# Optimization experiments

Hardware: AMD Instinct MI355X
Metric: run time of the kernel (lower is better)

Reference implementation:

```python
import jax, jax.numpy as jnp
import numpy as np

EMB, HEADS, LAT, FFN = 1024, 16, 256, 4096
HD = EMB // HEADS
B, N = 2, 2048

def _ln(x, w, b, eps=1e-5):
    mu = jnp.mean(x, axis=-1, keepdims=True)
    var = jnp.var(x, axis=-1, keepdims=True)
    return (x - mu) * jax.lax.rsqrt(var + eps) * w + b

def setup_inputs() -> dict:
    key = jax.random.key(0)
    ks = jax.random.split(key, 16)
    def lin(k, fan_in, fan_out):
        bound = 1.0 / np.sqrt(fan_in)
        kw, kb = jax.random.split(k)
        W = jax.random.uniform(kw, (fan_in, fan_out), jnp.float32, -bound, bound)
        b = jax.random.uniform(kb, (fan_out,), jnp.float32, -bound, bound)
        return W, b
    Wq, bq = lin(ks[0], EMB, EMB)
    WaK, baK = lin(ks[1], EMB, LAT)
    WbK, bbK = lin(ks[2], LAT, EMB)
    WaV, baV = lin(ks[3], EMB, LAT)
    WbV, bbV = lin(ks[4], LAT, EMB)
    Wo, bo = lin(ks[5], EMB, EMB)
    W1, b1 = lin(ks[6], EMB, FFN)
    W2, b2 = lin(ks[7], FFN, EMB)
    return {
        'x': jax.random.normal(ks[8], (B, N, EMB), jnp.float32),
        'attn_bias': jax.random.normal(ks[9], (N, N), jnp.float32),
        'Wq': Wq, 'bq': bq, 'WaK': WaK, 'baK': baK, 'WbK': WbK, 'bbK': bbK,
        'WaV': WaV, 'baV': baV, 'WbV': WbV, 'bbV': bbV, 'Wo': Wo, 'bo': bo,
        'W1': W1, 'b1': b1, 'W2': W2, 'b2': b2,
        'ln1_w': jnp.ones((EMB,), jnp.float32), 'ln1_b': jnp.zeros((EMB,), jnp.float32),
        'ln2_w': jnp.ones((EMB,), jnp.float32), 'ln2_b': jnp.zeros((EMB,), jnp.float32),
    }

def reference(x, attn_bias, Wq, bq, WaK, baK, WbK, bbK, WaV, baV, WbV, bbV,
              Wo, bo, W1, b1, W2, b2, ln1_w, ln1_b, ln2_w, ln2_b):
    Q = x @ Wq + bq                       # [B,N,E]
    K = (x @ WaK + baK) @ WbK + bbK       # low-rank K
    V = (x @ WaV + baV) @ WbV + bbV       # low-rank V
    def split(t):
        return t.reshape(B, N, HEADS, HD).transpose(0, 2, 1, 3)  # [B,H,N,D]
    Qh, Kh, Vh = split(Q), split(K), split(V)
    scores = jnp.einsum('bhnd,bhmd->bhnm', Qh, Kh) / np.sqrt(HD)
    scores = scores + attn_bias[None, None]
    weights = jax.nn.softmax(scores, axis=-1)
    attn = jnp.einsum('bhnm,bhmd->bhnd', weights, Vh)
    attn = attn.transpose(0, 2, 1, 3).reshape(B, N, EMB)
    attn = attn @ Wo + bo
    h = _ln(x + attn, ln1_w, ln1_b)
    ffn = jax.nn.gelu(h @ W1 + b1, approximate=False) @ W2 + b2
    return _ln(h + ffn, ln2_w, ln2_b)
```

## Files before the change

### kernel.cpp

```cpp
#include <hip/hip_runtime.h>
#include <hip/hip_bf16.h>
#include <math.h>

typedef unsigned short u16;
typedef short bf16x8 __attribute__((ext_vector_type(8)));
typedef float f32x4 __attribute__((ext_vector_type(4)));

#define EMB   1024
#define HEADS 16
#define HD    64
#define LATD  256
#define FFND  4096
#define BATCH 2
#define SEQ   2048
#define TOK   (BATCH*SEQ)

#define SCL2  0.18033688011112042f
#define LOG2E 1.4426950408889634f

__device__ __forceinline__ float bf2f(u16 u) {
    union { unsigned int i; float f; } x; x.i = ((unsigned int)u) << 16; return x.f;
}
__device__ __forceinline__ float bfLO(unsigned int u) {
    union { unsigned int i; float f; } x; x.i = u << 16; return x.f;
}
__device__ __forceinline__ float bfHI(unsigned int u) {
    union { unsigned int i; float f; } x; x.i = u & 0xffff0000u; return x.f;
}
__device__ __forceinline__ u16 f2bf(float f) {
    union { float f; unsigned int i; } x; x.f = f;
    unsigned int i = x.i;
    unsigned int lsb = (i >> 16) & 1u;
    i += 0x7fffu + lsb;
    return (u16)(i >> 16);
}
__device__ __forceinline__ void gld16(const u16* g, u16* l) {
    __builtin_amdgcn_global_load_lds(
        (const __attribute__((address_space(1))) void*)g,
        (__attribute__((address_space(3))) void*)l, 16, 0, 0);
}
__device__ __forceinline__ unsigned int cvt_pk_bf16(float a, float b) {
    unsigned int r;
    asm("v_cvt_pk_bf16_f32 %0, %1, %2" : "=v"(r) : "v"(a), "v"(b));
    return r;
}
#if defined(__has_builtin)
#if __has_builtin(__builtin_amdgcn_exp2f)
#define EXP2(x) __builtin_amdgcn_exp2f(x)
#endif
#endif
#ifndef EXP2
#define EXP2(x) exp2f(x)
#endif

struct TDesc { const float* src; u16* dst; int K; int N; int ofs; float scl; };
struct TTable { TDesc d[8]; };

struct PrepArgs {
    const float* x; u16* xb;
    const float* baK; const float* baV; const float* bq; float* bKV; float* bqs;
    const float* ab; u16* abP;
    TTable tt;
};

__global__ __launch_bounds__(256) void prep_all_kernel(PrepArgs pa)
{
    __shared__ u16 t[32][33];
    int blk = blockIdx.x;
    const int tid = threadIdx.x;

    if (blk < 2048) {
        int i = blk * 256 + tid;
        float4 f0 = *(const float4*)(pa.x + (size_t)i * 8);
        float4 f1 = *(const float4*)(pa.x + (size_t)i * 8 + 4);
        u16 e[8];
        e[0] = f2bf(f0.x); e[1] = f2bf(f0.y); e[2] = f2bf(f0.z); e[3] = f2bf(f0.w);
        e[4] = f2bf(f1.x); e[5] = f2bf(f1.y); e[6] = f2bf(f1.z); e[7] = f2bf(f1.w);
        *(uint4*)(pa.xb + (size_t)i * 8) = *(const uint4*)e;
        return;
    }
    blk -= 2048;
    if (blk < 6) {
        int i = blk * 256 + tid;
        if (i < 256)      pa.bKV[i] = pa.baK[i];
        else if (i < 512) pa.bKV[i] = pa.baV[i - 256];
        else              pa.bqs[i - 512] = pa.bq[i - 512] * SCL2;
        return;
    }
    blk -= 6;
    if (blk < 512) {
        const int kt = blk & 31, qt = blk >> 5;
        const int lane = tid & 63, wq = tid >> 6;
        const int qq = lane >> 4, col = lane & 15;
#pragma unroll
        for (int wi = wq; wi < 8; wi += 4)
#pragma unroll
            for (int mt = 0; mt < 4; mt++) {
                float4 v = *(const float4*)(pa.ab + (size_t)(qt * 128 + wi * 16 + col) * SEQ
                                            + kt * 64 + mt * 16 + qq * 4);
                uint2 pk;
                pk.x = cvt_pk_bf16(v.x * LOG2E, v.y * LOG2E);
                pk.y = cvt_pk_bf16(v.z * LOG2E, v.w * LOG2E);
                *(uint2*)(pa.abP + (((size_t)qt * 32 + kt) * 8 + wi) * 1024 + mt * 256 + lane * 4) = pk;
            }
        return;
    }
    blk -= 512;
    {
        int tb = blk, e = 0;
#pragma unroll
        for (int i = 1; i < 8; i++) if (tb >= pa.tt.d[i].ofs) e = i;
        const float* src = pa.tt.d[e].src;
        u16* dst = pa.tt.d[e].dst;
        const int K = pa.tt.d[e].K, N = pa.tt.d[e].N;
        const float scl = pa.tt.d[e].scl;
        const int local = tb - pa.tt.d[e].ofs;
        const int nx = N >> 5;
        const int bx = (local % nx) * 32;
        const int by = (local / nx) * 32;
        const int tx = tid & 31;
        const int ty = tid >> 5;
#pragma unroll
        for (int i = 0; i < 32; i += 8)
            t[ty + i][tx] = f2bf(src[(size_t)(by + ty + i) * N + bx + tx] * scl);
        __syncthreads();
#pragma unroll
        for (int i = 0; i < 32; i += 8)
            dst[(size_t)(bx + ty + i) * K + by + tx] = t[tx][ty + i];
    }
}

__device__ __forceinline__ void xcd_swz(int& bx, int& by)
{
    const int gx = gridDim.x;
    const int nwg = gx * gridDim.y;
    const int flat = blockIdx.x + gx * blockIdx.y;
    const int swz = (flat & 7) * (nwg >> 3) + (flat >> 3);
    bx = swz % gx;
    by = swz / gx;
}

#define BM 128
#define GBK 64

template <int ACT, int BNv, int TRC>
__device__ __forceinline__ void gemm_body(
    const u16* __restrict__ A, int lda, const u16* __restrict__ WT,
    const float* __restrict__ bias, u16* __restrict__ C,
    int K, int N, int bx, int by, u16* Al, u16* Wl, u16* Tl)
{
    const int NT = BNv / 32;
    const int WN = BNv / 2;
    const int CW = BNv / 32;

    const int tid  = threadIdx.x;
    const int lane = tid & 63;
    const int w    = tid >> 6;
    const int wm = w >> 1, wn = w & 1;
    const int col = lane & 15, qq = lane >> 4;
    const size_t bm = (size_t)by * BM;
    const size_t bn = (size_t)bx * BNv;

    f32x4 acc[4][NT];
#pragma unroll
    for (int mt = 0; mt < 4; mt++)
#pragma unroll
        for (int nt = 0; nt < NT; nt++) acc[mt][nt] = (f32x4){0.f, 0.f, 0.f, 0.f};

    const u16* gA[4]; u16* lA[4];
#pragma unroll
    for (int i = 0; i < 4; i++) {
        int f = w * 256 + i * 64 + lane;
        int r = f >> 3, s = f & 7, sg = s ^ (r & 7);
        gA[i] = A + (bm + r) * (size_t)lda + sg * 8;
        lA[i] = &Al[(size_t)(w * 256 + i * 64) * 8];
    }
    const u16* gW[4]; u16* lW[4];
#pragma unroll
    for (int i = 0; i < CW; i++) {
        int f = w * (BNv * 2) + i * 64 + lane;
        int r = f >> 3, s = f & 7, sg = s ^ (r & 7);
        gW[i] = WT + (bn + r) * (size_t)K + sg * 8;
        lW[i] = &Wl[(size_t)(w * (BNv * 2) + i * 64) * 8];
    }

    for (int k0 = 0; k0 < K; k0 += GBK) {
#pragma unroll
        for (int i = 0; i < 4; i++) gld16(gA[i] + k0, lA[i]);
#pragma unroll
        for (int i = 0; i < CW; i++) gld16(gW[i] + k0, lW[i]);
        __syncthreads();

#pragma unroll
        for (int kk = 0; kk < 2; kk++) {
            bf16x8 af[4], bfr[NT];
#pragma unroll
            for (int mt = 0; mt < 4; mt++) {
                int rr = wm * 64 + mt * 16 + col;
                int sub = (kk * 4 + qq) ^ (rr & 7);
                af[mt] = *(const bf16x8*)&Al[rr * GBK + sub * 8];
            }
#pragma unroll
            for (int nt = 0; nt < NT; nt++) {
                int rn = wn * WN + nt * 16 + col;
                int sub = (kk * 4 + qq) ^ (rn & 7);
                bfr[nt] = *(const bf16x8*)&Wl[rn * GBK + sub * 8];
            }
#pragma unroll
            for (int mt = 0; mt < 4; mt++)
#pragma unroll
                for (int nt = 0; nt < NT; nt++)
                    acc[mt][nt] = __builtin_amdgcn_mfma_f32_16x16x32_bf16(
                        af[mt], bfr[nt], acc[mt][nt], 0, 0, 0);
        }
        __syncthreads();
    }

    float bv[NT];
#pragma unroll
    for (int nt = 0; nt < NT; nt++)
        bv[nt] = bias[bn + wn * WN + nt * 16 + col];

    if (TRC) {
#pragma unroll
        for (int mt = 0; mt < 4; mt++)
#pragma unroll
            for (int nt = 0; nt < NT; nt++)
#pragma unroll
                for (int r = 0; r < 4; r++) {
                    float v = acc[mt][nt][r] + bv[nt];
                    Tl[(wn * WN + nt * 16 + col) * 136 + (wm * 64 + mt * 16 + qq * 4 + r)] = f2bf(v);
                }
        __syncthreads();
        const int b_ = (int)(bm >> 11);
        const size_t tokb = bm & (SEQ - 1);
        const int row = tid >> 2;
        u16* dst = C + ((size_t)b_ * EMB + (size_t)bx * 64 + row) * SEQ + tokb;
        const u16* srcl = Tl + row * 136;
#pragma unroll
        for (int j = 0; j < 4; j++) {
            int c0 = ((tid & 3) + j * 4) * 8;
            *(uint4*)(dst + c0) = *(const uint4*)(srcl + c0);
        }
        return;
    }

#pragma unroll
    for (int mt = 0; mt < 4; mt++) {
#pragma unroll
        for (int nt = 0; nt < NT; nt++) {
#pragma unroll
            for (int r = 0; r < 4; r++) {
                float v = acc[mt][nt][r] + bv[nt];
                if (ACT == 1) v = 0.5f * v * (1.0f + erff(v * 0.70710678118654752f));
                size_t rg = bm + wm * 64 + mt * 16 + qq * 4 + r;
                C[rg * (size_t)N + bn + wn * WN + nt * 16 + col] = f2bf(v);
            }
        }
    }
}

template <int ACT, int BNv, int MINW>
__global__ __launch_bounds__(256, MINW) void gemm_bt_kernel(
    const u16* __restrict__ A, int lda, const u16* __restrict__ WT,
    const float* __restrict__ bias, u16* __restrict__ C,
    int K, int N)
{
    __shared__ __align__(16) u16 Al[BM * GBK];
    __shared__ __align__(16) u16 Wl[BNv * GBK];
    int bx, by;
    xcd_swz(bx, by);
    gemm_body<ACT, BNv, 0>(A, lda, WT, bias, C, K, N, bx, by, Al, Wl, Al);
}

struct GPair {
    const u16* A0; const u16* A1;
    const u16* W0; const u16* W1;
    const float* b0; const float* b1;
    u16* C0; u16* C1;
    int lda0, lda1, N0, N1, nx0;
};

template <int BNv, int MINW, int TRV>
__global__ __launch_bounds__(256, MINW) void gemm_pair_kernel(GPair p, int K)
{
    __shared__ __align__(16) u16 SH[BM * GBK + BNv * GBK];
    u16* Al = SH;
    u16* Wl = SH + BM * GBK;
    int bxs, by;
    xcd_swz(bxs, by);
    const bool s1 = bxs >= p.nx0;
    const u16* A = s1 ? p.A1 : p.A0;
    const u16* WT = s1 ? p.W1 : p.W0;
    const float* bias = s1 ? p.b1 : p.b0;
    u16* C = s1 ? p.C1 : p.C0;
    const int lda = s1 ? p.lda1 : p.lda0;
    const int N = s1 ? p.N1 : p.N0;
    const int bx = s1 ? bxs - p.nx0 : bxs;
    if (TRV && s1)
        gemm_body<0, BNv, 1>(A, lda, WT, bias, C, K, N, bx, by, Al, Wl, SH);
    else
        gemm_body<0, BNv, 0>(A, lda, WT, bias, C, K, N, bx, by, Al, Wl, SH);
}

#define BQ   128
#define BKV  64
#define NKVT (SEQ / BKV)
#define LDP  72

__global__ __launch_bounds__(512, 4) void fattn_kernel(
    const u16* __restrict__ Q, const u16* __restrict__ K,
    const u16* __restrict__ VT, const u16* __restrict__ abP,
    u16* __restrict__ O)
{
    __shared__ __align__(16) u16 Ks[2][BKV * 64];
    __shared__ __align__(16) u16 Vt[2][HD * 64];
    __shared__ __align__(16) u16 Ps[BQ * LDP];

    const int tid = threadIdx.x;
    const int lane = tid & 63;
    const int w = tid >> 6;
    const int col = lane & 15, qq = lane >> 4;
    const int qt = blockIdx.x;
    const int b = blockIdx.y >> 4, h = blockIdx.y & 15;
    const size_t tok0 = (size_t)b * SEQ + (size_t)qt * BQ;
    const int wrow = w * 16;
    const size_t kvbase = (size_t)b * SEQ * EMB + h * HD;
    const size_t vtb = ((size_t)b * EMB + h * HD) * SEQ;

    const int krow = tid >> 3;
    const int kch  = tid & 7;
    const int kcol = kch * 8;
    const int ksw  = (kch ^ (krow & 7)) * 8;

    bf16x8 aq[2];
#pragma unroll
    for (int kk = 0; kk < 2; kk++)
        aq[kk] = *(const bf16x8*)(Q + (tok0 + wrow + col) * EMB + h * HD + kk * 32 + qq * 8);

    float m_st = -1e30f, l_st = 0.f;
    f32x4 o_acc[4];
#pragma unroll
    for (int dt = 0; dt < 4; dt++) o_acc[dt] = (f32x4){0.f, 0.f, 0.f, 0.f};

    const int c7 = col & 7;
    const int sw0 = (qq ^ c7) * 8;
    const int sw1 = ((4 + qq) ^ c7) * 8;

    uint4 kreg, vreg;
#define LOADKV(KV0) do {                                                              \
        kreg = *(const uint4*)(K + kvbase + (size_t)((KV0) + krow) * EMB + kcol);     \
        vreg = *(const uint4*)(VT + vtb + (size_t)krow * SEQ + (KV0) + kcol);         \
    } while (0)

    LOADKV(0);
    *(uint4*)&Ks[0][krow * 64 + ksw] = kreg;
    *(uint4*)&Vt[0][krow * 64 + ksw] = vreg;
    __syncthreads();
    LOADKV(BKV);

    const u16* abq = abP + (size_t)qt * NKVT * 8192 + (size_t)w * 1024;
    uint2 abr[4];
#pragma unroll
    for (int mt = 0; mt < 4; mt++)
        abr[mt] = *(const uint2*)(abq + mt * 256 + lane * 4);

    for (int t = 0; t < NKVT; t++) {
        const int cur = t & 1;
        const u16* Kc = Ks[cur];

        f32x4 s2[4];
#pragma unroll
        for (int mt = 0; mt < 4; mt++) {
            s2[mt][0] = bfLO(abr[mt].x);
            s2[mt][1] = bfHI(abr[mt].x);
            s2[mt][2] = bfLO(abr[mt].y);
            s2[mt][3] = bfHI(abr[mt].y);
        }
        __builtin_amdgcn_s_setprio(1);
#pragma unroll
        for (int mt = 0; mt < 4; mt++) {
            bf16x8 ak0 = *(const bf16x8*)&Kc[(mt * 16 + col) * 64 + sw0];
            bf16x8 ak1 = *(const bf16x8*)&Kc[(mt * 16 + col) * 64 + sw1];
            s2[mt] = __builtin_amdgcn_mfma_f32_16x16x32_bf16(ak0, aq[0], s2[mt], 0, 0, 0);
            s2[mt] = __builtin_amdgcn_mfma_f32_16x16x32_bf16(ak1, aq[1], s2[mt], 0, 0, 0);
        }
        __builtin_amdgcn_s_setprio(0);

        if (t + 1 < NKVT) {
            const u16* abn = abq + (size_t)(t + 1) * 8192;
#pragma unroll
            for (int mt = 0; mt < 4; mt++)
                abr[mt] = *(const uint2*)(abn + mt * 256 + lane * 4);
        }

        if (t + 1 < NKVT) {
            *(uint4*)&Ks[cur ^ 1][krow * 64 + ksw] = kreg;
            *(uint4*)&Vt[cur ^ 1][krow * 64 + ksw] = vreg;
        }
        if (t + 2 < NKVT) LOADKV((t + 2) * BKV);

        float t0 = fmaxf(fmaxf(s2[0][0], s2[0][1]), fmaxf(s2[0][2], s2[0][3]));
        float t1 = fmaxf(fmaxf(s2[1][0], s2[1][1]), fmaxf(s2[1][2], s2[1][3]));
        float t2 = fmaxf(fmaxf(s2[2][0], s2[2][1]), fmaxf(s2[2][2], s2[2][3]));
        float t3 = fmaxf(fmaxf(s2[3][0], s2[3][1]), fmaxf(s2[3][2], s2[3][3]));
        float tm = fmaxf(fmaxf(t0, t1), fmaxf(t2, t3));
        tm = fmaxf(tm, __shfl_xor(tm, 16));
        tm = fmaxf(tm, __shfl_xor(tm, 32));
        if (!__all(tm <= m_st + 8.f)) {
            float mnew = fmaxf(m_st, tm);
            float alpha = EXP2(m_st - mnew);
            m_st = mnew;
            l_st *= alpha;
#pragma unroll
            for (int dt = 0; dt < 4; dt++)
#pragma unroll
                for (int r = 0; r < 4; r++) o_acc[dt][r] *= alpha;
        }
        float rs = 0.f;
#pragma unroll
        for (int mt = 0; mt < 4; mt++)
#pragma unroll
            for (int r = 0; r < 4; r++) {
                float e = EXP2(s2[mt][r] - m_st);
                s2[mt][r] = e;
                rs += e;
            }
        rs += __shfl_xor(rs, 16);
        rs += __shfl_xor(rs, 32);
        l_st += rs;

#pragma unroll
        for (int mt = 0; mt < 4; mt++) {
            uint2 pp;
            pp.x = cvt_pk_bf16(s2[mt][0], s2[mt][1]);
            pp.y = cvt_pk_bf16(s2[mt][2], s2[mt][3]);
            *(uint2*)&Ps[(wrow + col) * LDP + mt * 16 + qq * 4] = pp;
        }

        __builtin_amdgcn_s_setprio(1);
#pragma unroll
        for (int kk = 0; kk < 2; kk++) {
            bf16x8 ap = *(const bf16x8*)&Ps[(wrow + col) * LDP + kk * 32 + qq * 8];
            const int swv = ((kk * 4 + qq) ^ c7) * 8;
#pragma unroll
            for (int dt = 0; dt < 4; dt++) {
                bf16x8 bv = *(const bf16x8*)&Vt[cur][(dt * 16 + col) * 64 + swv];
                o_acc[dt] = __builtin_amdgcn_mfma_f32_16x16x32_bf16(bv, ap, o_acc[dt], 0, 0, 0);
            }
        }
        __builtin_amdgcn_s_setprio(0);
        __syncthreads();
    }
#undef LOADKV

    float lr = 1.0f / l_st;
#pragma unroll
    for (int dt = 0; dt < 4; dt++) {
        uint2 pp;
        pp.x = cvt_pk_bf16(o_acc[dt][0] * lr, o_acc[dt][1] * lr);
        pp.y = cvt_pk_bf16(o_acc[dt][2] * lr, o_acc[dt][3] * lr);
        *(uint2*)(O + (tok0 + wrow + col) * EMB + h * HD + dt * 16 + qq * 4) = pp;
    }
}

template <int AF32, int OUTF32>
__global__ __launch_bounds__(256) void ln_kernel(
    const void* __restrict__ A, const u16* __restrict__ R,
    const float* __restrict__ w, const float* __restrict__ bb,
    void* __restrict__ out)
{
    __shared__ float r1[4], r2[4];
    const int tid = threadIdx.x;
    const size_t row = blockIdx.x;
    const int c0 = tid * 4;

    float v[4];
    {
        float a[4];
        if (AF32) {
            float4 av = *(const float4*)((const float*)A + row * EMB + c0);
            a[0] = av.x; a[1] = av.y; a[2] = av.z; a[3] = av.w;
        } else {
            ushort4 av = *(const ushort4*)((const u16*)A + row * EMB + c0);
            a[0] = bf2f(av.x); a[1] = bf2f(av.y); a[2] = bf2f(av.z); a[3] = bf2f(av.w);
        }
        ushort4 rv = *(const ushort4*)(R + row * EMB + c0);
        v[0] = a[0] + bf2f(rv.x); v[1] = a[1] + bf2f(rv.y);
        v[2] = a[2] + bf2f(rv.z); v[3] = a[3] + bf2f(rv.w);
    }
    float s = (v[0] + v[1]) + (v[2] + v[3]);
    float s2 = (v[0] * v[0] + v[1] * v[1]) + (v[2] * v[2] + v[3] * v[3]);

#pragma unroll
    for (int o = 32; o > 0; o >>= 1) {
        s  += __shfl_down(s, o);
        s2 += __shfl_down(s2, o);
    }
    if ((tid & 63) == 0) { r1[tid >> 6] = s; r2[tid >> 6] = s2; }
    __syncthreads();
    s  = r1[0] + r1[1] + r1[2] + r1[3];
    s2 = r2[0] + r2[1] + r2[2] + r2[3];

    float mu = s * (1.0f / EMB);
    float var = s2 * (1.0f / EMB) - mu * mu;
    float rs = rsqrtf(var + 1e-5f);

    float4 wv = *(const float4*)(w + c0);
    float4 bv = *(const float4*)(bb + c0);
    float y0 = (v[0] - mu) * rs * wv.x + bv.x;
    float y1 = (v[1] - mu) * rs * wv.y + bv.y;
    float y2 = (v[2] - mu) * rs * wv.z + bv.z;
    float y3 = (v[3] - mu) * rs * wv.w + bv.w;
    if (OUTF32) {
        *(float4*)((float*)out + row * EMB + c0) = make_float4(y0, y1, y2, y3);
    } else {
        ushort4 ov;
        ov.x = f2bf(y0); ov.y = f2bf(y1); ov.z = f2bf(y2); ov.w = f2bf(y3);
        *(ushort4*)((u16*)out + row * EMB + c0) = ov;
    }
}

extern "C" void kernel_launch(void* const* d_in, const int* in_sizes, int n_in,
                              void* d_out, int out_size, void* d_ws, size_t ws_size,
                              hipStream_t stream)
{
    const float* x    = (const float*)d_in[0];
    const float* ab   = (const float*)d_in[1];
    const float* Wq   = (const float*)d_in[2];
    const float* bq   = (const float*)d_in[3];
    const float* WaK  = (const float*)d_in[4];
    const float* baK  = (const float*)d_in[5];
    const float* WbK  = (const float*)d_in[6];
    const float* bbK  = (const float*)d_in[7];
    const float* WaV  = (const float*)d_in[8];
    const float* baV  = (const float*)d_in[9];
    const float* WbV  = (const float*)d_in[10];
    const float* bbV  = (const float*)d_in[11];
    const float* Wo   = (const float*)d_in[12];
    const float* bo   = (const float*)d_in[13];
    const float* W1   = (const float*)d_in[14];
    const float* b1   = (const float*)d_in[15];
    const float* W2   = (const float*)d_in[16];
    const float* b2   = (const float*)d_in[17];
    const float* ln1w = (const float*)d_in[18];
    const float* ln1b = (const float*)d_in[19];
    const float* ln2w = (const float*)d_in[20];
    const float* ln2b = (const float*)d_in[21];

    u16* w = (u16*)d_ws;
    size_t o = 0;
    u16* WqT  = w + o; o += (size_t)EMB * EMB;
    u16* WaKT = w + o; o += (size_t)EMB * LATD;
    u16* WaVT = w + o; o += (size_t)EMB * LATD;
    u16* WbKT = w + o; o += (size_t)LATD * EMB;
    u16* WbVT = w + o; o += (size_t)LATD * EMB;
    u16* WoT  = w + o; o += (size_t)EMB * EMB;
    u16* W1T  = w + o; o += (size_t)EMB * FFND;
    u16* W2T  = w + o; o += (size_t)FFND * EMB;
    u16* Qb   = w + o; o += (size_t)TOK * EMB;
    u16* Kb   = w + o; o += (size_t)TOK * EMB;
    u16* Vb   = w + o; o += (size_t)TOK * EMB;
    u16* aOb  = w + o; o += (size_t)TOK * EMB;
    u16* projb= w + o; o += (size_t)TOK * EMB;
    u16* hb   = w + o; o += (size_t)TOK * EMB;
    u16* xb   = w + o; o += (size_t)TOK * EMB;
    float* bKV = (float*)(w + o); o += 1024;
    float* bqs = (float*)(w + o); o += 2048;
    u16* abP = projb;
    u16* KVa = aOb;
    u16* f1  = Qb;
    u16* f2  = projb;

    dim3 blk(256);

    PrepArgs pa;
    pa.x = x; pa.xb = xb;
    pa.baK = baK; pa.baV = baV; pa.bq = bq; pa.bKV = bKV; pa.bqs = bqs;
    pa.ab = ab; pa.abP = abP;
    pa.tt.d[0] = {Wq,  WqT,  EMB,  EMB,  0,    SCL2};
    pa.tt.d[1] = {WaK, WaKT, EMB,  LATD, 1024, 1.0f};
    pa.tt.d[2] = {WaV, WaVT, EMB,  LATD, 1280, 1.0f};
    pa.tt.d[3] = {WbK, WbKT, LATD, EMB,  1536, 1.0f};
    pa.tt.d[4] = {WbV, WbVT, LATD, EMB,  1792, 1.0f};
    pa.tt.d[5] = {Wo,  WoT,  EMB,  EMB,  2048, 1.0f};
    pa.tt.d[6] = {W1,  W1T,  EMB,  FFND, 3072, 1.0f};
    pa.tt.d[7] = {W2,  W2T,  FFND, EMB,  7168, 1.0f};
    prep_all_kernel<<<dim3(13830), blk, 0, stream>>>(pa);

    {
        GPair p;
        p.A0 = xb;  p.A1 = xb;
        p.W0 = WqT; p.W1 = WaKT;
        p.b0 = bqs; p.b1 = bKV;
        p.C0 = Qb;  p.C1 = KVa;
        p.lda0 = EMB; p.lda1 = EMB;
        p.N0 = EMB; p.N1 = 512; p.nx0 = 16;
        gemm_pair_kernel<64, 3, 0><<<dim3(24, TOK / BM), blk, 0, stream>>>(p, EMB);
    }
    {
        GPair p;
        p.A0 = KVa;  p.A1 = KVa + LATD;
        p.W0 = WbKT; p.W1 = WbVT;
        p.b0 = bbK;  p.b1 = bbV;
        p.C0 = Kb;   p.C1 = Vb;
        p.lda0 = 512; p.lda1 = 512;
        p.N0 = EMB; p.N1 = EMB; p.nx0 = 16;
        gemm_pair_kernel<64, 3, 1><<<dim3(32, TOK / BM), blk, 0, stream>>>(p, LATD);
    }

    fattn_kernel<<<dim3(SEQ / BQ, BATCH * HEADS), dim3(512), 0, stream>>>(Qb, Kb, Vb, abP, aOb);

    gemm_bt_kernel<0,64,3><<<dim3(EMB / 64, TOK / BM), blk, 0, stream>>>(aOb, EMB, WoT, bo, projb, EMB, EMB);

    ln_kernel<1,0><<<dim3(TOK), blk, 0, stream>>>(x, projb, ln1w, ln1b, hb);

    gemm_bt_kernel<1,128,2><<<dim3(FFND / 128, TOK / BM), blk, 0, stream>>>(hb, EMB, W1T, b1, f1, EMB, FFND);
    gemm_bt_kernel<0,64,3><<<dim3(EMB / 64, TOK / BM), blk, 0, stream>>>(f1, FFND, W2T, b2, f2, FFND, EMB);

    ln_kernel<0,1><<<dim3(TOK), blk, 0, stream>>>(hb, f2, ln2w, ln2b, (float*)d_out);
}
```

Before: 361.7 us.

## Split flash attention over KV halves with a separate merge kernel

Adds a split-KV variant of the attention kernel. Each block handles half of the key/value tiles and writes unnormalised fp32 partial outputs plus the running max and sum. A new reduce kernel merges the two halves into bf16. This doubles the attention grid from 512 to 1024 blocks so the GPU is better filled, at the cost of extra fp32 traffic and one more launch. It is used only when the workspace is large enough, since it reuses the hb buffer and extra workspace space for the partials.

```diff
diff --git a/kernel.cpp b/kernel.cpp
--- a/kernel.cpp
+++ b/kernel.cpp
@@ -308,10 +308,12 @@
 #define NKVT (SEQ / BKV)
 #define LDP  72
 
+template <int SPLIT>
 __global__ __launch_bounds__(512, 4) void fattn_kernel(
     const u16* __restrict__ Q, const u16* __restrict__ K,
     const u16* __restrict__ VT, const u16* __restrict__ abP,
-    u16* __restrict__ O)
+    u16* __restrict__ O, float* __restrict__ Of0, float* __restrict__ Of1,
+    float* __restrict__ Ml)
 {
     __shared__ __align__(16) u16 Ks[2][BKV * 64];
     __shared__ __align__(16) u16 Vt[2][HD * 64];
@@ -323,6 +325,9 @@
     const int col = lane & 15, qq = lane >> 4;
     const int qt = blockIdx.x;
     const int b = blockIdx.y >> 4, h = blockIdx.y & 15;
+    const int zh = SPLIT ? (int)blockIdx.z : 0;
+    const int t0 = zh << 4;
+    const int NTL = SPLIT ? 16 : 32;
     const size_t tok0 = (size_t)b * SEQ + (size_t)qt * BQ;
     const int wrow = w * 16;
     const size_t kvbase = (size_t)b * SEQ * EMB + h * HD;
@@ -353,19 +358,19 @@
         vreg = *(const uint4*)(VT + vtb + (size_t)krow * SEQ + (KV0) + kcol);         \
     } while (0)
 
-    LOADKV(0);
+    LOADKV(t0 * BKV);
     *(uint4*)&Ks[0][krow * 64 + ksw] = kreg;
     *(uint4*)&Vt[0][krow * 64 + ksw] = vreg;
     __syncthreads();
-    LOADKV(BKV);
-
-    const u16* abq = abP + (size_t)qt * NKVT * 8192 + (size_t)w * 1024;
+    LOADKV((t0 + 1) * BKV);
+
+    const u16* abq = abP + ((size_t)qt * NKVT + t0) * 8192 + (size_t)w * 1024;
     uint2 abr[4];
 #pragma unroll
     for (int mt = 0; mt < 4; mt++)
         abr[mt] = *(const uint2*)(abq + mt * 256 + lane * 4);
 
-    for (int t = 0; t < NKVT; t++) {
+    for (int t = 0; t < NTL; t++) {
         const int cur = t & 1;
         const u16* Kc = Ks[cur];
 
@@ -387,24 +392,24 @@
         }
         __builtin_amdgcn_s_setprio(0);
 
-        if (t + 1 < NKVT) {
+        if (t + 1 < NTL) {
             const u16* abn = abq + (size_t)(t + 1) * 8192;
 #pragma unroll
             for (int mt = 0; mt < 4; mt++)
                 abr[mt] = *(const uint2*)(abn + mt * 256 + lane * 4);
         }
 
-        if (t + 1 < NKVT) {
+        if (t + 1 < NTL) {
             *(uint4*)&Ks[cur ^ 1][krow * 64 + ksw] = kreg;
             *(uint4*)&Vt[cur ^ 1][krow * 64 + ksw] = vreg;
         }
-        if (t + 2 < NKVT) LOADKV((t + 2) * BKV);
-
-        float t0 = fmaxf(fmaxf(s2[0][0], s2[0][1]), fmaxf(s2[0][2], s2[0][3]));
-        float t1 = fmaxf(fmaxf(s2[1][0], s2[1][1]), fmaxf(s2[1][2], s2[1][3]));
-        float t2 = fmaxf(fmaxf(s2[2][0], s2[2][1]), fmaxf(s2[2][2], s2[2][3]));
-        float t3 = fmaxf(fmaxf(s2[3][0], s2[3][1]), fmaxf(s2[3][2], s2[3][3]));
-        float tm = fmaxf(fmaxf(t0, t1), fmaxf(t2, t3));
+        if (t + 2 < NTL) LOADKV((t0 + t + 2) * BKV);
+
+        float t0_ = fmaxf(fmaxf(s2[0][0], s2[0][1]), fmaxf(s2[0][2], s2[0][3]));
+        float t1_ = fmaxf(fmaxf(s2[1][0], s2[1][1]), fmaxf(s2[1][2], s2[1][3]));
+        float t2_ = fmaxf(fmaxf(s2[2][0], s2[2][1]), fmaxf(s2[2][2], s2[2][3]));
+        float t3_ = fmaxf(fmaxf(s2[3][0], s2[3][1]), fmaxf(s2[3][2], s2[3][3]));
+        float tm = fmaxf(fmaxf(t0_, t1_), fmaxf(t2_, t3_));
         tm = fmaxf(tm, __shfl_xor(tm, 16));
         tm = fmaxf(tm, __shfl_xor(tm, 32));
         if (!__all(tm <= m_st + 8.f)) {
@@ -454,14 +459,50 @@
     }
 #undef LOADKV
 
-    float lr = 1.0f / l_st;
-#pragma unroll
-    for (int dt = 0; dt < 4; dt++) {
-        uint2 pp;
-        pp.x = cvt_pk_bf16(o_acc[dt][0] * lr, o_acc[dt][1] * lr);
-        pp.y = cvt_pk_bf16(o_acc[dt][2] * lr, o_acc[dt][3] * lr);
-        *(uint2*)(O + (tok0 + wrow + col) * EMB + h * HD + dt * 16 + qq * 4) = pp;
-    }
+    const size_t tokg = tok0 + wrow + col;
+    if (SPLIT) {
+        float* Ofh = zh ? Of1 : Of0;
+#pragma unroll
+        for (int dt = 0; dt < 4; dt++)
+            *(f32x4*)(Ofh + tokg * EMB + h * HD + dt * 16 + qq * 4) = o_acc[dt];
+        if (qq == 0)
+            ((float2*)Ml)[(size_t)zh * TOK * HEADS + tokg * HEADS + h] =
+                make_float2(m_st, l_st);
+    } else {
+        float lr = 1.0f / l_st;
+#pragma unroll
+        for (int dt = 0; dt < 4; dt++) {
+            uint2 pp;
+            pp.x = cvt_pk_bf16(o_acc[dt][0] * lr, o_acc[dt][1] * lr);
+            pp.y = cvt_pk_bf16(o_acc[dt][2] * lr, o_acc[dt][3] * lr);
+            *(uint2*)(O + tokg * EMB + h * HD + dt * 16 + qq * 4) = pp;
+        }
+    }
+}
+
+__global__ __launch_bounds__(256) void reduce_o_kernel(
+    const float* __restrict__ Of0, const float* __restrict__ Of1,
+    const float* __restrict__ Ml, u16* __restrict__ O)
+{
+    const int idx = blockIdx.x * 256 + threadIdx.x;
+    const int th = idx >> 4;
+    const int dg = (idx & 15) * 4;
+    const int tok = th >> 4, h = th & 15;
+
+    const float2* Ml2 = (const float2*)Ml;
+    float2 a = Ml2[th];
+    float2 c = Ml2[TOK * HEADS + th];
+    float m = fmaxf(a.x, c.x);
+    float w1 = EXP2(a.x - m), w2 = EXP2(c.x - m);
+    float inv = 1.0f / (a.y * w1 + c.y * w2);
+
+    const size_t base = (size_t)tok * EMB + h * HD + dg;
+    f32x4 o1 = *(const f32x4*)(Of0 + base);
+    f32x4 o2 = *(const f32x4*)(Of1 + base);
+    uint2 pp;
+    pp.x = cvt_pk_bf16((o1[0] * w1 + o2[0] * w2) * inv, (o1[1] * w1 + o2[1] * w2) * inv);
+    pp.y = cvt_pk_bf16((o1[2] * w1 + o2[2] * w2) * inv, (o1[3] * w1 + o2[3] * w2) * inv);
+    *(uint2*)(O + base) = pp;
 }
 
 template <int AF32, int OUTF32>
@@ -572,6 +613,12 @@
     u16* f1  = Qb;
     u16* f2  = projb;
 
+    float* Of0 = (float*)hb;
+    float* Of1 = (float*)(w + o);
+    float* Ml  = Of1 + (size_t)TOK * EMB;
+    const size_t need_bytes = o * 2 + ((size_t)TOK * EMB + (size_t)2 * TOK * HEADS * 2) * 4;
+    const bool split = ws_size >= need_bytes;
+
     dim3 blk(256);
 
     PrepArgs pa;
@@ -609,7 +656,14 @@
         gemm_pair_kernel<64, 3, 1><<<dim3(32, TOK / BM), blk, 0, stream>>>(p, LATD);
     }
 
-    fattn_kernel<<<dim3(SEQ / BQ, BATCH * HEADS), dim3(512), 0, stream>>>(Qb, Kb, Vb, abP, aOb);
+    if (split) {
+        fattn_kernel<1><<<dim3(SEQ / BQ, BATCH * HEADS, 2), dim3(512), 0, stream>>>(
+            Qb, Kb, Vb, abP, aOb, Of0, Of1, Ml);
+        reduce_o_kernel<<<dim3(TOK * HEADS * 16 / 256), blk, 0, stream>>>(Of0, Of1, Ml, aOb);
+    } else {
+        fattn_kernel<0><<<dim3(SEQ / BQ, BATCH * HEADS), dim3(512), 0, stream>>>(
+            Qb, Kb, Vb, abP, aOb, nullptr, nullptr, nullptr);
+    }
 
     gemm_bt_kernel<0,64,3><<<dim3(EMB / 64, TOK / BM), blk, 0, stream>>>(aOb, EMB, WoT, bo, projb, EMB, EMB);
 
```

Result: slower. 372.9 us (+3.1%).
